# Optimization experiments

Hardware: AMD Instinct MI355X
Metric: run time of the kernel (lower is better)

The kernel has to match this reference:

```python
import jax, jax.numpy as jnp
import numpy as np

EPS = 1e-5
R = 3


def _layernorm(x, gamma, beta):
    mu = jnp.mean(x, axis=-1, keepdims=True)
    var = jnp.mean(jnp.square(x - mu), axis=-1, keepdims=True)
    return (x - mu) * jax.lax.rsqrt(var + EPS) * gamma + beta


def setup_inputs() -> dict:
    key = jax.random.key(0)
    ks = jax.random.split(key, 16)
    N, C, H, W = 32, 256, 32, 32
    ic = C // 2
    L = H * W
    R2 = R * R
    d_attn = R2 * L        # 9216
    d_out = ic * L         # 131072
    return {
        "x": jax.random.normal(ks[0], (N, C, H, W), jnp.float32),
        "wq": jax.random.normal(ks[1], (ic, C), jnp.float32) / np.sqrt(C),
        "wk": jax.random.normal(ks[2], (ic, C), jnp.float32) / np.sqrt(C),
        "gamma1": jnp.ones((d_attn,), jnp.float32),
        "beta1": jnp.zeros((d_attn,), jnp.float32),
        "w1": jax.random.normal(ks[3], (C, d_attn), jnp.float32) / np.sqrt(d_attn),
        "b1": jnp.zeros((C,), jnp.float32),
        "w2": jax.random.normal(ks[4], (d_out, C), jnp.float32) / np.sqrt(C),
        "b2": jnp.zeros((d_out,), jnp.float32),
        "gamma2": jnp.ones((d_out,), jnp.float32),
        "beta2": jnp.zeros((d_out,), jnp.float32),
        "w_out": jax.random.normal(ks[5], (C, ic), jnp.float32) / np.sqrt(ic),
        "bn_gamma": jax.random.normal(ks[6], (C,), jnp.float32),
        "bn_beta": jax.random.normal(ks[7], (C,), jnp.float32),
        "bn_mean": jax.random.normal(ks[8], (C,), jnp.float32),
        "bn_var": jax.random.uniform(ks[9], (C,), jnp.float32, 0.5, 1.5),
    }


def reference(x, wq, wk, gamma1, beta1, w1, b1, w2, b2, gamma2, beta2,
              w_out, bn_gamma, bn_beta, bn_mean, bn_var):
    N, C, H, W = x.shape
    ic = wq.shape[0]
    L = H * W
    R2 = R * R
    pad = (R - 1) // 2

    # 1x1 convs == channel GEMMs
    q = jnp.einsum('nchw,oc->nohw', x, wq).reshape(N, ic, L)       # [N,ic,L]
    k = jnp.einsum('nchw,oc->nohw', x, wk)                          # [N,ic,H,W]

    # unfold: RxR local patches, torch channel-major ordering [ic, R2]
    kp = jnp.pad(k, ((0, 0), (0, 0), (pad, pad), (pad, pad)))
    patches = jnp.stack([kp[:, :, i:i + H, j:j + W]
                         for i in range(R) for j in range(R)], axis=-1)
    patches = patches.reshape(N, ic, L, R2)                         # [N,ic,L,R2]

    # local attention scores: q . k over channels at each spatial loc
    f = jnp.einsum('ncl,nclr->nlr', q, patches)                     # [N,L,R2]
    f = f.transpose(0, 2, 1).reshape(N, R2 * L)                     # [N, R2*L]

    # f = f + dropout(f) -> identity at inference => 2f
    f = f + f
    f = _layernorm(f, gamma1, beta1)

    # FFN
    h = jax.nn.relu(f @ w1.T + b1)                                  # [N,C]
    h = h @ w2.T + b2                                               # [N, ic*L]
    h = _layernorm(h, gamma2, beta2)
    y = h.reshape(N, ic, H, W)

    # output 1x1 conv + BatchNorm2d (inference mode)
    wy = jnp.einsum('nchw,oc->nohw', y, w_out)                      # [N,C,H,W]
    scale = (bn_gamma * jax.lax.rsqrt(bn_var + EPS))[None, :, None, None]
    wy = (wy - bn_mean[None, :, None, None]) * scale + bn_beta[None, :, None, None]
    return wy + x
```

## Files before the change

kernel.cpp:

```cpp
#include <hip/hip_runtime.h>

#define NN 32
#define CC 256
#define LL 1024
#define IC 128
#define DA 9216
#define DOUT 131072
#define EPSF 1e-5f

typedef __attribute__((ext_vector_type(8))) short short8;
typedef __attribute__((ext_vector_type(4))) float f32x4;

__device__ __forceinline__ ushort bf_rne(float f) {
  union { float f; unsigned u; } v;
  v.f = f;
  unsigned u = v.u;
  u += 0x7FFF + ((u >> 16) & 1);
  return (ushort)(u >> 16);
}

__device__ __forceinline__ unsigned bfp2(float lo, float hi) {
  union { float f; unsigned u; } a, b;
  a.f = lo; b.f = hi;
  return __builtin_amdgcn_perm(b.u + 0x8000u, a.u + 0x8000u, 0x07060302u);
}

__global__ __launch_bounds__(256) void k_wcvt(const float* __restrict__ wq,
                                              const float* __restrict__ wk,
                                              const float* __restrict__ wo,
                                              ushort* __restrict__ wqkbf,
                                              ushort* __restrict__ wobf,
                                              float* __restrict__ fz) {
  int b = blockIdx.x;
  if (b < 96) {
    int idx = (b * 256 + threadIdx.x) * 4;
    float4 v;
    if (idx < 32768) v = *(const float4*)(wq + idx);
    else if (idx < 65536) v = *(const float4*)(wk + idx - 32768);
    else v = *(const float4*)(wo + idx - 65536);
    uint2 o;
    o.x = bfp2(v.x, v.y);
    o.y = bfp2(v.z, v.w);
    if (idx < 65536) *(uint2*)(wqkbf + idx) = o;
    else *(uint2*)(wobf + idx - 65536) = o;
  } else {
    int idx = ((b - 96) * 256 + threadIdx.x) * 4;
    if (idx < 294976)
      *(float4*)(fz + idx) = make_float4(0.f, 0.f, 0.f, 0.f);
  }
}

__global__ __launch_bounds__(256, 4) void k_qkx(const float* __restrict__ x,
                                                const ushort* __restrict__ wqkbf,
                                                float* __restrict__ q,
                                                float* __restrict__ k) {
  __shared__ ushort xl[64 * 264];
  int t = threadIdx.x;
  int n = blockIdx.y;
  int l0 = blockIdx.x * 64;
  int lane = t & 63, wv = t >> 6;
  int m16 = lane & 15, kg = lane >> 4;

  {
    int l = t & 63, g = t >> 6;
    const float* xn = x + ((size_t)n * CC) * LL + l0 + l;
#pragma unroll
    for (int i = 0; i < 8; i++) {
      int c8 = (i * 4 + g) * 8;
      float v[8];
#pragma unroll
      for (int j = 0; j < 8; j++) v[j] = xn[(size_t)(c8 + j) * LL];
      union { short8 s; unsigned u[4]; } p;
      p.u[0] = bfp2(v[0], v[1]);
      p.u[1] = bfp2(v[2], v[3]);
      p.u[2] = bfp2(v[4], v[5]);
      p.u[3] = bfp2(v[6], v[7]);
      *(short8*)&xl[l * 264 + c8] = p.s;
    }
  }
  __syncthreads();

  f32x4 acc[2][2][4];
#pragma unroll
  for (int mt = 0; mt < 2; mt++)
#pragma unroll
    for (int ms = 0; ms < 2; ms++)
#pragma unroll
      for (int ls = 0; ls < 4; ls++) acc[mt][ms][ls] = (f32x4){0.f, 0.f, 0.f, 0.f};

#pragma unroll
  for (int kc = 0; kc < 8; kc++) {
    short8 a[2][2];
#pragma unroll
    for (int mt = 0; mt < 2; mt++)
#pragma unroll
      for (int ms = 0; ms < 2; ms++)
        a[mt][ms] = *(const short8*)(wqkbf +
            (((mt * 128 + wv * 32 + ms * 16 + m16) << 8) + kc * 32 + kg * 8));
#pragma unroll
    for (int ls = 0; ls < 4; ls++) {
      short8 b = *(const short8*)&xl[(ls * 16 + m16) * 264 + kc * 32 + kg * 8];
      acc[0][0][ls] =
          __builtin_amdgcn_mfma_f32_16x16x32_bf16(a[0][0], b, acc[0][0][ls], 0, 0, 0);
      acc[0][1][ls] =
          __builtin_amdgcn_mfma_f32_16x16x32_bf16(a[0][1], b, acc[0][1][ls], 0, 0, 0);
      acc[1][0][ls] =
          __builtin_amdgcn_mfma_f32_16x16x32_bf16(a[1][0], b, acc[1][0][ls], 0, 0, 0);
      acc[1][1][ls] =
          __builtin_amdgcn_mfma_f32_16x16x32_bf16(a[1][1], b, acc[1][1][ls], 0, 0, 0);
    }
  }

#pragma unroll
  for (int mt = 0; mt < 2; mt++) {
    float* outp = (mt ? k : q) + (size_t)n * IC * LL;
#pragma unroll
    for (int ms = 0; ms < 2; ms++)
#pragma unroll
      for (int ls = 0; ls < 4; ls++) {
        int col = l0 + ls * 16 + m16;
#pragma unroll
        for (int r = 0; r < 4; r++)
          outp[(size_t)(wv * 32 + ms * 16 + kg * 4 + r) * LL + col] =
              acc[mt][ms][ls][r];
      }
  }
}

__global__ __launch_bounds__(256) void k_attn(const float* __restrict__ q,
                                              const float* __restrict__ k,
                                              float* __restrict__ f2) {
  int n = blockIdx.x;
  int c0 = blockIdx.y * 32;
  int l = blockIdx.z * 256 + threadIdx.x;
  int h = l >> 5, w = l & 31;
  const float* qn = q + (size_t)n * IC * LL;
  const float* kn = k + (size_t)n * IC * LL;
  bool val[9];
  int off[9];
#pragma unroll
  for (int i = 0; i < 3; i++)
#pragma unroll
    for (int j = 0; j < 3; j++) {
      int r = i * 3 + j;
      int hh = h + i - 1, ww = w + j - 1;
      val[r] = (hh >= 0 && hh < 32 && ww >= 0 && ww < 32);
      off[r] = hh * 32 + ww;
    }
  float acc[9];
#pragma unroll
  for (int r = 0; r < 9; r++) acc[r] = 0.f;
#pragma unroll 4
  for (int cc = 0; cc < 32; cc++) {
    int c = c0 + cc;
    float qv = qn[c * LL + l];
    const float* kc = kn + c * LL;
#pragma unroll
    for (int r = 0; r < 9; r++) {
      float kv = val[r] ? kc[off[r]] : 0.f;
      acc[r] += qv * kv;
    }
  }
#pragma unroll
  for (int r = 0; r < 9; r++)
    atomicAdd(&f2[(size_t)n * DA + r * LL + l], 2.f * acc[r]);
}

__global__ __launch_bounds__(256) void k_ln1(float* __restrict__ f2,
                                             const float* __restrict__ g1,
                                             const float* __restrict__ b1) {
  int n = blockIdx.x, t = threadIdx.x;
  float* row = f2 + (size_t)n * DA;
  float4 v[9];
  float s = 0.f, ss = 0.f;
#pragma unroll
  for (int kk = 0; kk < 9; kk++) {
    v[kk] = ((const float4*)row)[t + kk * 256];
    s += v[kk].x + v[kk].y + v[kk].z + v[kk].w;
    ss += v[kk].x * v[kk].x + v[kk].y * v[kk].y + v[kk].z * v[kk].z +
          v[kk].w * v[kk].w;
  }
#pragma unroll
  for (int o = 32; o; o >>= 1) {
    s += __shfl_down(s, o);
    ss += __shfl_down(ss, o);
  }
  __shared__ float ps[4], pss[4], stats[2];
  int wid = t >> 6, lid = t & 63;
  if (lid == 0) { ps[wid] = s; pss[wid] = ss; }
  __syncthreads();
  if (t == 0) {
    float S = ps[0] + ps[1] + ps[2] + ps[3];
    float SS = pss[0] + pss[1] + pss[2] + pss[3];
    float mu = S / DA;
    float var = SS / DA - mu * mu;
    stats[0] = mu;
    stats[1] = rsqrtf(var + EPSF);
  }
  __syncthreads();
  float mu = stats[0], rs = stats[1];
#pragma unroll
  for (int kk = 0; kk < 9; kk++) {
    float4 g = ((const float4*)g1)[t + kk * 256];
    float4 b = ((const float4*)b1)[t + kk * 256];
    float4 o;
    o.x = (v[kk].x - mu) * rs * g.x + b.x;
    o.y = (v[kk].y - mu) * rs * g.y + b.y;
    o.z = (v[kk].z - mu) * rs * g.z + b.z;
    o.w = (v[kk].w - mu) * rs * g.w + b.w;
    ((float4*)row)[t + kk * 256] = o;
  }
}

__global__ __launch_bounds__(256) void k_ffn1(const float* __restrict__ fln,
                                              const float* __restrict__ w1,
                                              const float* __restrict__ b1,
                                              ushort* __restrict__ h1bf) {
  int o = blockIdx.x, nsb = blockIdx.y * 16, t = threadIdx.x;
  float acc[16];
#pragma unroll
  for (int i = 0; i < 16; i++) acc[i] = 0.f;
  const float4* w1r = (const float4*)(w1 + (size_t)o * DA);
  for (int kk = 0; kk < 9; kk++) {
    float4 wv = w1r[t + kk * 256];
#pragma unroll
    for (int i = 0; i < 16; i++) {
      float4 fv = ((const float4*)(fln + (size_t)(nsb + i) * DA))[t + kk * 256];
      acc[i] += wv.x * fv.x + wv.y * fv.y + wv.z * fv.z + wv.w * fv.w;
    }
  }
#pragma unroll
  for (int i = 0; i < 16; i++)
#pragma unroll
    for (int s = 32; s; s >>= 1) acc[i] += __shfl_down(acc[i], s);
  __shared__ float part[4][16];
  int wid = t >> 6, lid = t & 63;
  if (lid == 0) {
#pragma unroll
    for (int i = 0; i < 16; i++) part[wid][i] = acc[i];
  }
  __syncthreads();
  if (t < 16) {
    float sum = part[0][t] + part[1][t] + part[2][t] + part[3][t] + b1[o];
    h1bf[(size_t)(nsb + t) * CC + o] = bf_rne(fmaxf(sum, 0.f));
  }
}

__global__ __launch_bounds__(256, 4) void k_ffn2(
    const ushort* __restrict__ h1bf, const float* __restrict__ w2,
    const float* __restrict__ b2, float* __restrict__ h2,
    float* __restrict__ st) {
  __shared__ float bs[64];
  int t = threadIdx.x;
  int lane = t & 63, wv = t >> 6;
  int m16 = lane & 15, kg = lane >> 4;
  int j0 = blockIdx.x * 128 + wv * 32;
  if (t < 64) bs[t] = 0.f;

  int j[2] = {j0 + m16, j0 + 16 + m16};

  f32x4 acc[2][2];
#pragma unroll
  for (int m = 0; m < 2; m++)
#pragma unroll
    for (int nn = 0; nn < 2; nn++) acc[m][nn] = (f32x4){0.f, 0.f, 0.f, 0.f};

  float4 lo[2], hi[2];
#pragma unroll
  for (int nn = 0; nn < 2; nn++) {
    const float* src = w2 + (size_t)j[nn] * CC + kg * 8;
    lo[nn] = *(const float4*)src;
    hi[nn] = *(const float4*)(src + 4);
  }

#pragma unroll
  for (int kc = 0; kc < 8; kc++) {
    short8 a0 = *(const short8*)(h1bf + m16 * CC + kc * 32 + kg * 8);
    short8 a1 = *(const short8*)(h1bf + (16 + m16) * CC + kc * 32 + kg * 8);
    short8 bf[2];
#pragma unroll
    for (int nn = 0; nn < 2; nn++) {
      union { short8 s; unsigned u[4]; } cv;
      cv.u[0] = bfp2(lo[nn].x, lo[nn].y);
      cv.u[1] = bfp2(lo[nn].z, lo[nn].w);
      cv.u[2] = bfp2(hi[nn].x, hi[nn].y);
      cv.u[3] = bfp2(hi[nn].z, hi[nn].w);
      bf[nn] = cv.s;
    }
    if (kc < 7) {
#pragma unroll
      for (int nn = 0; nn < 2; nn++) {
        const float* src = w2 + (size_t)j[nn] * CC + (kc + 1) * 32 + kg * 8;
        lo[nn] = *(const float4*)src;
        hi[nn] = *(const float4*)(src + 4);
      }
    }
#pragma unroll
    for (int nn = 0; nn < 2; nn++) {
      acc[0][nn] =
          __builtin_amdgcn_mfma_f32_16x16x32_bf16(a0, bf[nn], acc[0][nn], 0, 0, 0);
      acc[1][nn] =
          __builtin_amdgcn_mfma_f32_16x16x32_bf16(a1, bf[nn], acc[1][nn], 0, 0, 0);
    }
  }
  __syncthreads();

  float b2v[2] = {b2[j[0]], b2[j[1]]};

  float s8[2][4], q8[2][4];
#pragma unroll
  for (int m = 0; m < 2; m++)
#pragma unroll
    for (int r = 0; r < 4; r++) { s8[m][r] = 0.f; q8[m][r] = 0.f; }
#pragma unroll
  for (int m = 0; m < 2; m++)
#pragma unroll
    for (int nn = 0; nn < 2; nn++) {
#pragma unroll
      for (int r = 0; r < 4; r++) {
        float v = acc[m][nn][r] + b2v[nn];
        int row = m * 16 + kg * 4 + r;
        h2[(size_t)row * DOUT + j[nn]] = v;
        s8[m][r] += v;
        q8[m][r] += v * v;
      }
    }
#pragma unroll
  for (int off = 8; off; off >>= 1)
#pragma unroll
    for (int m = 0; m < 2; m++)
#pragma unroll
      for (int r = 0; r < 4; r++) {
        s8[m][r] += __shfl_down(s8[m][r], off, 16);
        q8[m][r] += __shfl_down(q8[m][r], off, 16);
      }
  if (m16 == 0) {
#pragma unroll
    for (int m = 0; m < 2; m++)
#pragma unroll
      for (int r = 0; r < 4; r++) {
        int row = m * 16 + kg * 4 + r;
        atomicAdd(&bs[row], s8[m][r]);
        atomicAdd(&bs[32 + row], q8[m][r]);
      }
  }
  __syncthreads();
  if (t < 64) atomicAdd(&st[t], bs[t]);
}

__global__ __launch_bounds__(256, 4) void k_out(
    const float* __restrict__ h2, const float* __restrict__ st,
    const float* __restrict__ g2, const float* __restrict__ b2,
    const ushort* __restrict__ wobf, const float* __restrict__ bn_g,
    const float* __restrict__ bn_b, const float* __restrict__ bn_m,
    const float* __restrict__ bn_v, const float* __restrict__ x,
    float* __restrict__ out) {
  __shared__ ushort yl[32 * 136];
  int t = threadIdx.x;
  int n = blockIdx.y;
  int l0 = blockIdx.x * 32;
  float mu = st[n] * (1.f / DOUT);
  float rs = rsqrtf(st[32 + n] * (1.f / DOUT) - mu * mu + EPSF);

  {
    int l = t & 31, og = t >> 5;
    const float* h2n = h2 + (size_t)n * DOUT;
#pragma unroll
    for (int half = 0; half < 2; half++) {
      float y[8];
#pragma unroll
      for (int jj = 0; jj < 8; jj++) {
        int o = og * 16 + half * 8 + jj;
        int d = o * LL + l0 + l;
        y[jj] = (h2n[d] - mu) * rs * g2[d] + b2[d];
      }
      union { short8 s; unsigned u[4]; } p;
      p.u[0] = bfp2(y[0], y[1]);
      p.u[1] = bfp2(y[2], y[3]);
      p.u[2] = bfp2(y[4], y[5]);
      p.u[3] = bfp2(y[6], y[7]);
      *(short8*)&yl[l * 136 + og * 16 + half * 8] = p.s;
    }
  }
  __syncthreads();

  int lane = t & 63, wv = t >> 6;
  int m16 = lane & 15, kg = lane >> 4;
  f32x4 acc[4][2];
#pragma unroll
  for (int ms = 0; ms < 4; ms++)
#pragma unroll
    for (int ls = 0; ls < 2; ls++) acc[ms][ls] = (f32x4){0.f, 0.f, 0.f, 0.f};

#pragma unroll
  for (int kc = 0; kc < 4; kc++) {
    short8 b[2];
#pragma unroll
    for (int ls = 0; ls < 2; ls++)
      b[ls] = *(const short8*)&yl[(ls * 16 + m16) * 136 + kc * 32 + kg * 8];
#pragma unroll
    for (int ms = 0; ms < 4; ms++) {
      short8 a = *(const short8*)(wobf +
          (((wv * 64 + ms * 16 + m16) << 7) + kc * 32 + kg * 8));
#pragma unroll
      for (int ls = 0; ls < 2; ls++)
        acc[ms][ls] =
            __builtin_amdgcn_mfma_f32_16x16x32_bf16(a, b[ls], acc[ms][ls], 0, 0, 0);
    }
  }

#pragma unroll
  for (int ms = 0; ms < 4; ms++)
#pragma unroll
    for (int r = 0; r < 4; r++) {
      int O = wv * 64 + ms * 16 + kg * 4 + r;
      float sc = bn_g[O] * rsqrtf(bn_v[O] + EPSF);
      float sh = bn_b[O] - bn_m[O] * sc;
#pragma unroll
      for (int ls = 0; ls < 2; ls++) {
        int col = l0 + ls * 16 + m16;
        size_t base = ((size_t)(n * CC + O)) * LL + col;
        out[base] = acc[ms][ls][r] * sc + sh + x[base];
      }
    }
}

extern "C" void kernel_launch(void* const* d_in, const int* in_sizes, int n_in,
                              void* d_out, int out_size, void* d_ws,
                              size_t ws_size, hipStream_t stream) {
  const float* x = (const float*)d_in[0];
  const float* wq = (const float*)d_in[1];
  const float* wk = (const float*)d_in[2];
  const float* gamma1 = (const float*)d_in[3];
  const float* beta1 = (const float*)d_in[4];
  const float* w1 = (const float*)d_in[5];
  const float* b1 = (const float*)d_in[6];
  const float* w2 = (const float*)d_in[7];
  const float* b2 = (const float*)d_in[8];
  const float* gamma2 = (const float*)d_in[9];
  const float* beta2 = (const float*)d_in[10];
  const float* w_out = (const float*)d_in[11];
  const float* bn_g = (const float*)d_in[12];
  const float* bn_b = (const float*)d_in[13];
  const float* bn_m = (const float*)d_in[14];
  const float* bn_v = (const float*)d_in[15];
  float* outp = (float*)d_out;
  float* ws = (float*)d_ws;

  float* qb = ws;
  float* kb = ws + 4194304;
  float* fb = ws + 8388608;
  float* stb = ws + 8683520;
  ushort* h1bfb = (ushort*)(ws + 8683584);
  ushort* wqkbfb = (ushort*)(ws + 8687680);
  ushort* wobfb = (ushort*)(ws + 8720448);
  float* h2b = qb;

  if (ws_size < 8736832ull * sizeof(float)) return;

  k_wcvt<<<dim3(385), 256, 0, stream>>>(wq, wk, w_out, wqkbfb, wobfb, fb);
  k_qkx<<<dim3(16, 32), 256, 0, stream>>>(x, wqkbfb, qb, kb);
  k_attn<<<dim3(32, 4, 4), 256, 0, stream>>>(qb, kb, fb);
  k_ln1<<<dim3(32), 256, 0, stream>>>(fb, gamma1, beta1);
  k_ffn1<<<dim3(256, 2), 256, 0, stream>>>(fb, w1, b1, h1bfb);
  k_ffn2<<<dim3(1024), 256, 0, stream>>>(h1bfb, w2, b2, h2b, stb);
  k_out<<<dim3(32, 32), 256, 0, stream>>>(h2b, stb, gamma2, beta2, wobfb,
                                          bn_g, bn_b, bn_m, bn_v, x, outp);
}
```

Baseline: 345.1 us.

## Stage w2 tile in LDS as bf16 with coalesced loads in ffn2

The ffn2 kernel now loads its whole 128x256 fp32 w2 tile with fully coalesced float4 loads (32 in flight per thread), converts it to bf16, and stores it in padded shared memory. The MFMA B operands are then read from LDS instead of from per-lane strided global loads interleaved with compute. This targets the main cost of the kernel, which is streaming the 134MB w2 matrix at good bandwidth. In exchange it uses about 67KB of LDS per block and lowers the launch-bounds occupancy hint from 4 to 2, so fewer blocks may be resident to hide latency.

```diff
diff --git a/kernel.cpp b/kernel.cpp
--- a/kernel.cpp
+++ b/kernel.cpp
@@ -246,64 +246,63 @@
   }
 }
 
-__global__ __launch_bounds__(256, 4) void k_ffn2(
+__global__ __launch_bounds__(256, 2) void k_ffn2(
     const ushort* __restrict__ h1bf, const float* __restrict__ w2,
     const float* __restrict__ b2, float* __restrict__ h2,
     float* __restrict__ st) {
+  __shared__ ushort wt[128 * 264];
   __shared__ float bs[64];
   int t = threadIdx.x;
+  int j0 = blockIdx.x * 128;
+  if (t < 64) bs[t] = 0.f;
+
+  {
+    const float* wsrc = w2 + (size_t)j0 * CC;
+    int row_t = t >> 6;
+    int col_t = (t & 63) * 4;
+#pragma unroll
+    for (int io = 0; io < 4; io++) {
+      float4 v[8];
+#pragma unroll
+      for (int u = 0; u < 8; u++)
+        v[u] = *(const float4*)(wsrc + (size_t)(io * 8 + u) * 1024 + t * 4);
+#pragma unroll
+      for (int u = 0; u < 8; u++) {
+        int row = (io * 8 + u) * 4 + row_t;
+        uint2 p;
+        p.x = bfp2(v[u].x, v[u].y);
+        p.y = bfp2(v[u].z, v[u].w);
+        *(uint2*)&wt[row * 264 + col_t] = p;
+      }
+    }
+  }
+  __syncthreads();
+
   int lane = t & 63, wv = t >> 6;
   int m16 = lane & 15, kg = lane >> 4;
-  int j0 = blockIdx.x * 128 + wv * 32;
-  if (t < 64) bs[t] = 0.f;
-
-  int j[2] = {j0 + m16, j0 + 16 + m16};
+  int jw = j0 + wv * 32;
+  int j[2] = {jw + m16, jw + 16 + m16};
 
   f32x4 acc[2][2];
 #pragma unroll
   for (int m = 0; m < 2; m++)
 #pragma unroll
     for (int nn = 0; nn < 2; nn++) acc[m][nn] = (f32x4){0.f, 0.f, 0.f, 0.f};
-
-  float4 lo[2], hi[2];
-#pragma unroll
-  for (int nn = 0; nn < 2; nn++) {
-    const float* src = w2 + (size_t)j[nn] * CC + kg * 8;
-    lo[nn] = *(const float4*)src;
-    hi[nn] = *(const float4*)(src + 4);
-  }
 
 #pragma unroll
   for (int kc = 0; kc < 8; kc++) {
     short8 a0 = *(const short8*)(h1bf + m16 * CC + kc * 32 + kg * 8);
     short8 a1 = *(const short8*)(h1bf + (16 + m16) * CC + kc * 32 + kg * 8);
-    short8 bf[2];
 #pragma unroll
     for (int nn = 0; nn < 2; nn++) {
-      union { short8 s; unsigned u[4]; } cv;
-      cv.u[0] = bfp2(lo[nn].x, lo[nn].y);
-      cv.u[1] = bfp2(lo[nn].z, lo[nn].w);
-      cv.u[2] = bfp2(hi[nn].x, hi[nn].y);
-      cv.u[3] = bfp2(hi[nn].z, hi[nn].w);
-      bf[nn] = cv.s;
-    }
-    if (kc < 7) {
-#pragma unroll
-      for (int nn = 0; nn < 2; nn++) {
-        const float* src = w2 + (size_t)j[nn] * CC + (kc + 1) * 32 + kg * 8;
-        lo[nn] = *(const float4*)src;
-        hi[nn] = *(const float4*)(src + 4);
-      }
-    }
-#pragma unroll
-    for (int nn = 0; nn < 2; nn++) {
+      short8 b = *(const short8*)&wt[(wv * 32 + nn * 16 + m16) * 264 +
+                                     kc * 32 + kg * 8];
       acc[0][nn] =
-          __builtin_amdgcn_mfma_f32_16x16x32_bf16(a0, bf[nn], acc[0][nn], 0, 0, 0);
+          __builtin_amdgcn_mfma_f32_16x16x32_bf16(a0, b, acc[0][nn], 0, 0, 0);
       acc[1][nn] =
-          __builtin_amdgcn_mfma_f32_16x16x32_bf16(a1, bf[nn], acc[1][nn], 0, 0, 0);
-    }
-  }
-  __syncthreads();
+          __builtin_amdgcn_mfma_f32_16x16x32_bf16(a1, b, acc[1][nn], 0, 0, 0);
+    }
+  }
 
   float b2v[2] = {b2[j[0]], b2[j[1]]};
 
```

Result: no change. 343.1 us (-0.6%).
